# Kernel tuning notes

Measured on AMD Instinct MI355X. Metric: run time of the kernel, lower is better.

Reference implementation:

```python
import jax, jax.numpy as jnp
import numpy as np

SHIFT = 1  # torch module picks shift_direction in {-1,+1} randomly; fixed to +1 for determinism
K = 9      # unfold kernel height
PAD = 4    # unfold padding along H


def setup_inputs() -> dict:
    key = jax.random.key(0)
    k1, k2, k3 = jax.random.split(key, 3)
    x = jax.random.normal(k1, (1, 24, 56, 56), dtype=jnp.float32)
    w0 = jax.random.normal(k2, (96, 9, 14), dtype=jnp.float32)   # weights[0]
    w1 = jax.random.normal(k3, (24, 2, 14), dtype=jnp.float32)   # weights[1]
    return {"x": x, "w0": w0, "w1": w1}


def reference(x, w0, w1):
    # einsum 'limn, ikj -> lmnkj': (1,24,56,56) x (24,2,14) -> (1,56,56,2,14)
    t = jnp.einsum('limn,ikj->lmnkj', x, w1)
    # view as NCHW with C=56, H=56, W=28 for unfold(kernel=(9,1), padding=(4,0))
    t = t.reshape(1, 56, 56, 28)
    tp = jnp.pad(t, ((0, 0), (0, 0), (PAD, PAD), (0, 0)))
    # unfold along H: windows[:, c, kh, h, w] = padded[:, c, h + kh, w]
    win = jnp.stack([tp[:, :, i:i + 56, :] for i in range(K)], axis=2)  # (1,56,9,56,28)
    # merge (56,2) -> 112 (last 28 = 2*14), roll along that merged axis, split back, sum over the 2-axis
    t = win.reshape(1, 56, K, 112, 14)
    t = jnp.roll(t, SHIFT, axis=3)
    t = t.reshape(1, 56, K, 56, 2, 14).sum(axis=4)  # (1,56,9,56,14)
    # einsum 'lmjnk, ijk -> limn': (1,56,9,56,14) x (96,9,14) -> (1,96,56,56)
    return jnp.einsum('lmjnk,ijk->limn', t, w0)
```

## Files before the change

### kernel.cpp

```cpp
#include <hip/hip_runtime.h>


#define MDIM 56
#define NDIM 56
#define CIN  24
#define JD   14
#define KJD  28
#define KHD  9
#define IOUT 96
#define ITILE 24
#define TIL 3
#define TNN 2

__global__ __launch_bounds__(256) void fused_shift_conv(
    const float* __restrict__ x,
    const float* __restrict__ w0,
    const float* __restrict__ w1,
    float* __restrict__ out)
{
    const int m     = blockIdx.x;
    const int itile = blockIdx.y;
    const int tid   = threadIdx.x;

    __shared__ __align__(16) float sx [CIN * MDIM];
    __shared__ __align__(16) float sw1[CIN * KJD];
    __shared__ __align__(16) float sw0[ITILE * KHD * JD];
    __shared__ __align__(16) float sB [64 * KJD];
    __shared__ __align__(16) float sS [KHD * NDIM * JD];

    {
        float4*       sx4  = (float4*)sx;
        float4*       sw14 = (float4*)sw1;
        float4*       sw04 = (float4*)sw0;
        float4*       sB4  = (float4*)sB;
        const float4* x4   = (const float4*)x;
        const float4* w14  = (const float4*)w1;
        const float4* w04  = (const float4*)w0;

        for (int e = tid; e < CIN * JD; e += 256) {
            int c = e / JD, t = e % JD;
            sx4[e] = x4[c * 784 + m * JD + t];
        }
        for (int e = tid; e < (CIN * KJD) / 4; e += 256)
            sw14[e] = w14[e];
        for (int e = tid; e < (ITILE * KHD * JD) / 4; e += 256)
            sw04[e] = w04[itile * (ITILE * KHD * JD / 4) + e];
        for (int e = tid; e < 56; e += 256) {
            int r = e / 7;
            int hp = r + (r >= 4 ? 56 : 0);
            sB4[hp * 7 + (e % 7)] = make_float4(0.f, 0.f, 0.f, 0.f);
        }
    }
    __syncthreads();

    if (tid < 196) {
        const int g   = tid / 7;
        const int q   = tid % 7;
        const int h0  = 2 * g;
        const int kj0 = 4 * q;

        float4 acc0 = make_float4(0.f, 0.f, 0.f, 0.f);
        float4 acc1 = make_float4(0.f, 0.f, 0.f, 0.f);
        #pragma unroll
        for (int c = 0; c < CIN; ++c) {
            float2 xv = *(const float2*)&sx[c * MDIM + h0];
            float4 wv = *(const float4*)&sw1[c * KJD + kj0];
            acc0.x += xv.x * wv.x;  acc0.y += xv.x * wv.y;
            acc0.z += xv.x * wv.z;  acc0.w += xv.x * wv.w;
            acc1.x += xv.y * wv.x;  acc1.y += xv.y * wv.y;
            acc1.z += xv.y * wv.z;  acc1.w += xv.y * wv.w;
        }
        *(float4*)&sB[(h0 + 4) * KJD + kj0] = acc0;
        *(float4*)&sB[(h0 + 5) * KJD + kj0] = acc1;
    }
    __syncthreads();

    for (int e = tid; e < KHD * NDIM * 7; e += 256) {
        int kh = e / (NDIM * 7);
        int r  = e % (NDIM * 7);
        int n  = r / 7;
        int j2 = 2 * (r % 7);
        int h1 = (n + 55) % 56;
        float2 a = *(const float2*)&sB[(n  + kh) * KJD + j2];
        float2 b = *(const float2*)&sB[(h1 + kh) * KJD + JD + j2];
        *(float2*)&sS[(kh * NDIM + n) * JD + j2] = make_float2(a.x + b.x, a.y + b.y);
    }
    __syncthreads();

    if (tid < (ITILE / TIL) * (NDIM / TNN)) {
        const int il0 = TIL * (tid % (ITILE / TIL));
        const int n0  = TNN * (tid / (ITILE / TIL));

        float acc[TIL][TNN] = {};

        #pragma unroll
        for (int kh = 0; kh < KHD; ++kh) {
            const float2* s0 = (const float2*)&sS[(kh * NDIM + n0    ) * JD];
            const float2* s1 = (const float2*)&sS[(kh * NDIM + n0 + 1) * JD];
            const float2* wa = (const float2*)&sw0[((il0 + 0) * KHD + kh) * JD];
            const float2* wb = (const float2*)&sw0[((il0 + 1) * KHD + kh) * JD];
            const float2* wc = (const float2*)&sw0[((il0 + 2) * KHD + kh) * JD];
            #pragma unroll
            for (int j2 = 0; j2 < 7; ++j2) {
                float2 v0 = s0[j2], v1 = s1[j2];
                float2 A = wa[j2], B = wb[j2], C = wc[j2];
                acc[0][0] += A.x * v0.x + A.y * v0.y;
                acc[0][1] += A.x * v1.x + A.y * v1.y;
                acc[1][0] += B.x * v0.x + B.y * v0.y;
                acc[1][1] += B.x * v1.x + B.y * v1.y;
                acc[2][0] += C.x * v0.x + C.y * v0.y;
                acc[2][1] += C.x * v1.x + C.y * v1.y;
            }
        }

        #pragma unroll
        for (int a = 0; a < TIL; ++a) {
            int i = itile * ITILE + il0 + a;
            *(float2*)&out[(i * MDIM + m) * NDIM + n0] =
                make_float2(acc[a][0], acc[a][1]);
        }
    }
}

extern "C" void kernel_launch(void* const* d_in, const int* in_sizes, int n_in,
                              void* d_out, int out_size, void* d_ws, size_t ws_size,
                              hipStream_t stream) {
    const float* x  = (const float*)d_in[0];
    const float* w0 = (const float*)d_in[1];
    const float* w1 = (const float*)d_in[2];
    float* out = (float*)d_out;

    dim3 grid(MDIM, IOUT / ITILE);
    dim3 block(256);
    fused_shift_conv<<<grid, block, 0, stream>>>(x, w0, w1, out);
}
```

Measured before the change: 64.33 us.

## Double block size and split kh reduction across two thread halves

Raises the block from 256 to 512 threads. The first GEMM stage now uses 392 threads with two-column outputs instead of 196 threads with four. The final contraction over kh is split between the two halves (kh 0-4 and 5-8). The second half writes its partial sums to reused shared memory, and after a barrier the first half adds them and stores the output. The intent is to cut per-thread serial work and latency in this small grid of 224 blocks, at the cost of an extra barrier, a shared-memory round trip, and possibly lower occupancy per CU.

```diff
diff --git a/kernel.cpp b/kernel.cpp
--- a/kernel.cpp
+++ b/kernel.cpp
@@ -9,10 +9,9 @@
 #define KHD  9
 #define IOUT 96
 #define ITILE 24
-#define TIL 3
-#define TNN 2
+#define NT   512
 
-__global__ __launch_bounds__(256) void fused_shift_conv(
+__global__ __launch_bounds__(NT) void fused_shift_conv(
     const float* __restrict__ x,
     const float* __restrict__ w0,
     const float* __restrict__ w1,
@@ -37,15 +36,15 @@
         const float4* w14  = (const float4*)w1;
         const float4* w04  = (const float4*)w0;
 
-        for (int e = tid; e < CIN * JD; e += 256) {
+        for (int e = tid; e < CIN * JD; e += NT) {
             int c = e / JD, t = e % JD;
             sx4[e] = x4[c * 784 + m * JD + t];
         }
-        for (int e = tid; e < (CIN * KJD) / 4; e += 256)
+        for (int e = tid; e < (CIN * KJD) / 4; e += NT)
             sw14[e] = w14[e];
-        for (int e = tid; e < (ITILE * KHD * JD) / 4; e += 256)
+        for (int e = tid; e < (ITILE * KHD * JD) / 4; e += NT)
             sw04[e] = w04[itile * (ITILE * KHD * JD / 4) + e];
-        for (int e = tid; e < 56; e += 256) {
+        for (int e = tid; e < 56; e += NT) {
             int r = e / 7;
             int hp = r + (r >= 4 ? 56 : 0);
             sB4[hp * 7 + (e % 7)] = make_float4(0.f, 0.f, 0.f, 0.f);
@@ -53,29 +52,25 @@
     }
     __syncthreads();
 
-    if (tid < 196) {
-        const int g   = tid / 7;
-        const int q   = tid % 7;
-        const int h0  = 2 * g;
-        const int kj0 = 4 * q;
+    if (tid < 392) {
+        const int h0  = 2 * (tid / 14);
+        const int kj0 = 2 * (tid % 14);
 
-        float4 acc0 = make_float4(0.f, 0.f, 0.f, 0.f);
-        float4 acc1 = make_float4(0.f, 0.f, 0.f, 0.f);
+        float2 acc0 = make_float2(0.f, 0.f);
+        float2 acc1 = make_float2(0.f, 0.f);
         #pragma unroll
         for (int c = 0; c < CIN; ++c) {
             float2 xv = *(const float2*)&sx[c * MDIM + h0];
-            float4 wv = *(const float4*)&sw1[c * KJD + kj0];
+            float2 wv = *(const float2*)&sw1[c * KJD + kj0];
             acc0.x += xv.x * wv.x;  acc0.y += xv.x * wv.y;
-            acc0.z += xv.x * wv.z;  acc0.w += xv.x * wv.w;
             acc1.x += xv.y * wv.x;  acc1.y += xv.y * wv.y;
-            acc1.z += xv.y * wv.z;  acc1.w += xv.y * wv.w;
         }
-        *(float4*)&sB[(h0 + 4) * KJD + kj0] = acc0;
-        *(float4*)&sB[(h0 + 5) * KJD + kj0] = acc1;
+        *(float2*)&sB[(h0 + 4) * KJD + kj0] = acc0;
+        *(float2*)&sB[(h0 + 5) * KJD + kj0] = acc1;
     }
     __syncthreads();
 
-    for (int e = tid; e < KHD * NDIM * 7; e += 256) {
+    for (int e = tid; e < KHD * NDIM * 7; e += NT) {
         int kh = e / (NDIM * 7);
         int r  = e % (NDIM * 7);
         int n  = r / 7;
@@ -87,14 +82,16 @@
     }
     __syncthreads();
 
-    if (tid < (ITILE / TIL) * (NDIM / TNN)) {
-        const int il0 = TIL * (tid % (ITILE / TIL));
-        const int n0  = TNN * (tid / (ITILE / TIL));
+    const int half = tid >> 8;
+    const int t    = tid & 255;
+    float* spart = sx;
 
-        float acc[TIL][TNN] = {};
+    float acc[3][2] = {{0.f,0.f},{0.f,0.f},{0.f,0.f}};
+    const int il0 = 3 * (t % 8);
+    const int n0  = 2 * (t / 8);
 
-        #pragma unroll
-        for (int kh = 0; kh < KHD; ++kh) {
+    if (t < 224) {
+        auto body = [&](int kh) {
             const float2* s0 = (const float2*)&sS[(kh * NDIM + n0    ) * JD];
             const float2* s1 = (const float2*)&sS[(kh * NDIM + n0 + 1) * JD];
             const float2* wa = (const float2*)&sw0[((il0 + 0) * KHD + kh) * JD];
@@ -111,13 +108,29 @@
                 acc[2][0] += C.x * v0.x + C.y * v0.y;
                 acc[2][1] += C.x * v1.x + C.y * v1.y;
             }
+        };
+        if (half == 0) {
+            #pragma unroll
+            for (int kh = 0; kh < 5; ++kh) body(kh);
+        } else {
+            #pragma unroll
+            for (int kh = 5; kh < 9; ++kh) body(kh);
+            float2* sp2 = (float2*)&spart[t * 6];
+            sp2[0] = make_float2(acc[0][0], acc[0][1]);
+            sp2[1] = make_float2(acc[1][0], acc[1][1]);
+            sp2[2] = make_float2(acc[2][0], acc[2][1]);
         }
+    }
+    __syncthreads();
 
+    if (half == 0 && t < 224) {
+        const float2* sp2 = (const float2*)&spart[t * 6];
         #pragma unroll
-        for (int a = 0; a < TIL; ++a) {
+        for (int a = 0; a < 3; ++a) {
+            float2 p = sp2[a];
             int i = itile * ITILE + il0 + a;
             *(float2*)&out[(i * MDIM + m) * NDIM + n0] =
-                make_float2(acc[a][0], acc[a][1]);
+                make_float2(acc[a][0] + p.x, acc[a][1] + p.y);
         }
     }
 }
@@ -131,6 +144,6 @@
     float* out = (float*)d_out;
 
     dim3 grid(MDIM, IOUT / ITILE);
-    dim3 block(256);
+    dim3 block(NT);
     fused_shift_conv<<<grid, block, 0, stream>>>(x, w0, w1, out);
 }
```

Result: no change. 63.26 us (-1.7%).
